# Kernel optimization log

Measured on AMD Instinct MI355X. Metric: run time of the kernel, lower is better.

Reference implementation:

```python
import jax, jax.numpy as jnp
import numpy as np

Q, N_EMBED, DIM = 4, 1024, 256
B, S = 8, 2048


def setup_inputs() -> dict:
    key = jax.random.key(0)
    k1, k2 = jax.random.split(key)
    x = jax.random.normal(k1, (B, S, DIM), dtype=jnp.float32)
    codebooks = jax.random.normal(k2, (Q, N_EMBED, DIM), dtype=jnp.float32)
    return {"x": x, "codebooks": codebooks}


def _vq_lookup(flat, embed):
    # flat: [M, D], embed: [K, D]
    dist = (jnp.sum(flat * flat, axis=-1, keepdims=True)
            - 2.0 * flat @ embed.T
            + jnp.sum(embed * embed, axis=-1))
    idx = jnp.argmin(dist, axis=-1)          # [M]
    quantize = embed[idx]                    # gather: [M, D]
    return quantize, idx


def reference(x, codebooks):
    sg = jax.lax.stop_gradient
    b, s, d = x.shape
    num_q = codebooks.shape[0]
    residual = x
    quantized_output = jnp.zeros_like(x)
    all_indices, all_losses = [], []
    for i in range(num_q):  # small fixed loop over quantizers
        flat = residual.reshape(-1, d)
        q, idx = _vq_lookup(flat, codebooks[i])
        q = q.reshape(b, s, d)
        # commitment loss: mse(sg(quantize), input)
        loss = jnp.mean((sg(q) - residual) ** 2)
        # straight-through estimator
        q_st = residual + sg(q - residual)
        residual = residual - q_st
        quantized_output = quantized_output + q_st
        all_indices.append(idx.reshape(b, s))
        all_losses.append(loss)
    return quantized_output, jnp.stack(all_indices), jnp.stack(all_losses)
```

## Files before the change

kernel.cpp:

```cpp
#include <hip/hip_runtime.h>

#define QQ   4
#define NE   1024
#define DIMD 256
#define MM   16384
#define TM   32
#define NW   16
#define CAP  32

typedef short v8s __attribute__((ext_vector_type(8)));
typedef float v4f __attribute__((ext_vector_type(4)));


__device__ __forceinline__ unsigned short f2bf(float f) {
  unsigned u = __float_as_uint(f);
  return (unsigned short)((u + 0x7FFFu + ((u >> 16) & 1u)) >> 16);
}

__device__ __forceinline__ float np_sumsq_256_x32(const float* __restrict__ p,
                                                  int j) {
  const int bi = j >> 4, L = j & 15;
  const float* q = p + bi * 128 + L;
  float s0 = __fmul_rn(q[0], q[0]);
  float s1 = __fmul_rn(q[16], q[16]);
  float s2 = __fmul_rn(q[32], q[32]);
  float s3 = __fmul_rn(q[48], q[48]);
  float s4 = __fmul_rn(q[64], q[64]);
  float s5 = __fmul_rn(q[80], q[80]);
  float s6 = __fmul_rn(q[96], q[96]);
  float s7 = __fmul_rn(q[112], q[112]);
  float w = __fadd_rn(__fadd_rn(__fadd_rn(s0, s1), __fadd_rn(s2, s3)),
                      __fadd_rn(__fadd_rn(s4, s5), __fadd_rn(s6, s7)));
  float u  = __fadd_rn(w,  __shfl_down(w, 8, 64));
  float t  = __fadd_rn(u,  __shfl_down(u, 4, 64));
  float r2 = __fadd_rn(t,  __shfl_down(t, 2, 64));
  float bb = __fadd_rn(r2, __shfl_down(r2, 1, 64));
  return __fadd_rn(bb, __shfl_down(bb, 16, 64));
}

__device__ __forceinline__ float np_dist_f4(const float* __restrict__ xp,
                                            const float* __restrict__ ep,
                                            float a, float b) {
  float m = 0.f;
  #pragma unroll 16
  for (int d4 = 0; d4 < DIMD / 4; ++d4) {
    const float4 xv = *(const float4*)(xp + d4 * 4);
    const float4 ev = *(const float4*)(ep + d4 * 4);
    m = fmaf(xv.x, ev.x, m);
    m = fmaf(xv.y, ev.y, m);
    m = fmaf(xv.z, ev.z, m);
    m = fmaf(xv.w, ev.w, m);
  }
  return __fadd_rn(__fsub_rn(a, __fmul_rn(2.0f, m)), b);
}

__global__ __launch_bounds__(256) void k_prep(const float* __restrict__ cb,
                                              unsigned short* __restrict__ cb16,
                                              float* __restrict__ bK,
                                              double* __restrict__ lossP,
                                              unsigned* __restrict__ done) {
  const int g = blockIdx.x * 256 + threadIdx.x;
  {
    const int i = g * 4;
    float4 f = *(const float4*)(cb + i);
    unsigned short t[4] = {f2bf(f.x), f2bf(f.y), f2bf(f.z), f2bf(f.w)};
    *(short4*)(cb16 + i) = *(short4*)t;
  }
  if (g < QQ * NE * 32) {
    const int row = g >> 5, j = g & 31;
    float b = np_sumsq_256_x32(cb + (size_t)row * DIMD, j);
    if (j == 0) bK[row] = b;
  }
  if (g < QQ * 64) lossP[g] = 0.0;
  if (g == 0) *done = 0u;
}

__global__ __launch_bounds__(1024, 4) void k_fused(
    const float* __restrict__ x,
    const unsigned short* __restrict__ cb16a,
    const float* __restrict__ cba,
    const float* __restrict__ bKa,
    double* __restrict__ lossP,
    unsigned* __restrict__ doneCnt,
    float* __restrict__ out_q,
    float* __restrict__ idx_out,
    float* __restrict__ out_loss) {
  __shared__ float residF[TM][DIMD + 4];
  __shared__ unsigned short sX[TM][DIMD + 8];
  __shared__ float  sBK[NE];
  __shared__ float  av_s[TM];
  __shared__ float  candD[TM][NW];
  __shared__ float  thrS[TM];
  __shared__ int    cnt[TM];
  __shared__ int    candL[TM][CAP];
  __shared__ float  dcD[TM][CAP];
  __shared__ int    bcode[TM];
  __shared__ float  fwD[NW];
  __shared__ int    fwI[NW];
  __shared__ double lossW[NW];

  const int tid  = threadIdx.x;
  const int lane = tid & 63;
  const int wv   = tid >> 6;
  const int rowBase = blockIdx.x * TM;
  const int r32 = tid >> 5;
  const int j32 = tid & 31;
  const int d0  = j32 * 8;
  const int m16  = lane & 15;
  const int quad = lane >> 4;

  {
    const float* xp = x + (size_t)(rowBase + r32) * DIMD + d0;
    *(float4*)&residF[r32][d0]     = *(const float4*)xp;
    *(float4*)&residF[r32][d0 + 4] = *(const float4*)(xp + 4);
  }
  __syncthreads();

  #pragma unroll 1
  for (int qi = 0; qi < QQ; ++qi) {
    const unsigned short* cb16 = cb16a + (size_t)qi * NE * DIMD;
    const float* cb = cba + (size_t)qi * NE * DIMD;
    const float* bK = bKa + (size_t)qi * NE;

    {
      float av = np_sumsq_256_x32(&residF[r32][0], j32);
      if (j32 == 0) av_s[r32] = av;
    }
    if (tid < TM) cnt[tid] = 0;
    if (tid < NE) sBK[tid] = bK[tid];
    {
      const float* rp = &residF[r32][d0];
      const float4 f0 = *(const float4*)rp;
      const float4 f1 = *(const float4*)(rp + 4);
      unsigned short t[8] = {f2bf(f0.x), f2bf(f0.y), f2bf(f0.z), f2bf(f0.w),
                             f2bf(f1.x), f2bf(f1.y), f2bf(f1.z), f2bf(f1.w)};
      *(v8s*)&sX[r32][d0] = *(v8s*)t;
    }
    __syncthreads();

    float bmx;
    {
      float bm = sBK[lane];
      #pragma unroll
      for (int t = 1; t < 16; ++t) bm = fmaxf(bm, sBK[lane + t * 64]);
      #pragma unroll
      for (int off = 32; off; off >>= 1) bm = fmaxf(bm, __shfl_xor(bm, off, 64));
      bmx = bm;
    }

    v4f acc[2][4];
    #pragma unroll
    for (int mt = 0; mt < 2; ++mt)
      #pragma unroll
      for (int ct = 0; ct < 4; ++ct) acc[mt][ct] = (v4f)(0.f);
    const unsigned short* bptr =
        cb16 + ((size_t)(wv * 64 + m16)) * DIMD + quad * 8;
    #pragma unroll
    for (int kc = 0; kc < 8; ++kc) {
      v8s bfr[4];
      #pragma unroll
      for (int ct = 0; ct < 4; ++ct)
        bfr[ct] = *(const v8s*)(bptr + (size_t)ct * 16 * DIMD + kc * 32);
      v8s a0 = *(const v8s*)&sX[m16][kc * 32 + quad * 8];
      v8s a1 = *(const v8s*)&sX[16 + m16][kc * 32 + quad * 8];
      #pragma unroll
      for (int ct = 0; ct < 4; ++ct) {
        acc[0][ct] = __builtin_amdgcn_mfma_f32_16x16x32_bf16(a0, bfr[ct], acc[0][ct], 0, 0, 0);
        acc[1][ct] = __builtin_amdgcn_mfma_f32_16x16x32_bf16(a1, bfr[ct], acc[1][ct], 0, 0, 0);
      }
    }

    float av8[2][4];
    #pragma unroll
    for (int mt = 0; mt < 2; ++mt)
      #pragma unroll
      for (int v = 0; v < 4; ++v) av8[mt][v] = av_s[mt * 16 + quad * 4 + v];
    #pragma unroll
    for (int ct = 0; ct < 4; ++ct) {
      const float bv = sBK[wv * 64 + ct * 16 + m16];
      #pragma unroll
      for (int mt = 0; mt < 2; ++mt)
        #pragma unroll
        for (int v = 0; v < 4; ++v)
          acc[mt][ct][v] = av8[mt][v] - 2.0f * acc[mt][ct][v] + bv;
    }

    #pragma unroll
    for (int mt = 0; mt < 2; ++mt) {
      float vmin[4];
      #pragma unroll
      for (int v = 0; v < 4; ++v) {
        vmin[v] = acc[mt][0][v];
        #pragma unroll
        for (int ct = 1; ct < 4; ++ct) vmin[v] = fminf(vmin[v], acc[mt][ct][v]);
        #pragma unroll
        for (int off = 1; off < 16; off <<= 1)
          vmin[v] = fminf(vmin[v], __shfl_xor(vmin[v], off, 64));
      }
      if (m16 == 0) {
        #pragma unroll
        for (int v = 0; v < 4; ++v) candD[mt * 16 + quad * 4 + v][wv] = vmin[v];
      }
    }
    __syncthreads();
    if (tid < TM) {
      float bd = candD[tid][0];
      #pragma unroll
      for (int w = 1; w < NW; ++w) bd = fminf(bd, candD[tid][w]);
      thrS[tid] = bd + 0.03125f * sqrtf(av_s[tid] * bmx) + 0.1f;
    }
    __syncthreads();

    #pragma unroll
    for (int ct = 0; ct < 4; ++ct) {
      const int code = wv * 64 + ct * 16 + m16;
      #pragma unroll
      for (int mt = 0; mt < 2; ++mt) {
        #pragma unroll
        for (int v = 0; v < 4; ++v) {
          const int row = mt * 16 + quad * 4 + v;
          if (acc[mt][ct][v] <= thrS[row]) {
            int pos = atomicAdd(&cnt[row], 1);
            if (pos < CAP) candL[row][pos] = code;
          }
        }
      }
    }
    __syncthreads();

    {
      const int n = (cnt[r32] <= CAP) ? cnt[r32] : 0;
      if (j32 < n) {
        const int code = candL[r32][j32];
        dcD[r32][j32] = np_dist_f4(&residF[r32][0], cb + (size_t)code * DIMD,
                                   av_s[r32], sBK[code]);
      }
    }
    __syncthreads();

    for (int r = 0; r < TM; ++r) {
      if (cnt[r] > CAP) {
        const float* xp = &residF[r][0];
        const float a = av_s[r];
        float d1 = np_dist_f4(xp, cb + (size_t)tid * DIMD, a, sBK[tid]);
        int i1 = tid;
        #pragma unroll
        for (int off = 32; off; off >>= 1) {
          float vd = __shfl_xor(d1, off, 64);
          int vi = __shfl_xor(i1, off, 64);
          if (vd < d1 || (vd == d1 && vi < i1)) { d1 = vd; i1 = vi; }
        }
        if (lane == 0) { fwD[wv] = d1; fwI[wv] = i1; }
        __syncthreads();
        if (tid == 0) {
          float bd = fwD[0];
          int bi = fwI[0];
          #pragma unroll
          for (int w = 1; w < NW; ++w) {
            if (fwD[w] < bd || (fwD[w] == bd && fwI[w] < bi)) {
              bd = fwD[w]; bi = fwI[w];
            }
          }
          bcode[r] = bi;
        }
        __syncthreads();
      }
    }

    if (tid < TM) {
      if (cnt[tid] <= CAP) {
        float bd = 3.4e38f;
        int bi = 0x7fffffff;
        for (int ci = 0; ci < cnt[tid]; ++ci) {
          float d = dcD[tid][ci];
          int code = candL[tid][ci];
          if (d < bd || (d == bd && code < bi)) { bd = d; bi = code; }
        }
        bcode[tid] = bi;
      }
      idx_out[(size_t)qi * MM + rowBase + tid] = (float)bcode[tid];
    }
    __syncthreads();

    const int codeB = bcode[r32];
    double lsum = 0.0;
    #pragma unroll
    for (int h = 0; h < 2; ++h) {
      const int d = d0 + h * 4;
      const float4 ev = *(const float4*)(cb + (size_t)codeB * DIMD + d);
      const float4 rv = *(const float4*)&residF[r32][d];
      float t0 = __fsub_rn(ev.x, rv.x), u0 = __fadd_rn(rv.x, t0);
      float t1 = __fsub_rn(ev.y, rv.y), u1 = __fadd_rn(rv.y, t1);
      float t2 = __fsub_rn(ev.z, rv.z), u2 = __fadd_rn(rv.z, t2);
      float t3 = __fsub_rn(ev.w, rv.w), u3 = __fadd_rn(rv.w, t3);
      *(float4*)&residF[r32][d] =
          make_float4(__fsub_rn(rv.x, u0), __fsub_rn(rv.y, u1),
                      __fsub_rn(rv.z, u2), __fsub_rn(rv.w, u3));
      lsum += (double)__fmul_rn(t0, t0) + (double)__fmul_rn(t1, t1) +
              (double)__fmul_rn(t2, t2) + (double)__fmul_rn(t3, t3);
    }
    #pragma unroll
    for (int off = 32; off; off >>= 1) lsum += __shfl_xor(lsum, off, 64);
    if (lane == 0) lossW[wv] = lsum;
    __syncthreads();
    if (tid == 0) {
      double s = 0.0;
      #pragma unroll
      for (int w = 0; w < NW; ++w) s += lossW[w];
      atomicAdd(lossP + (size_t)qi * 64 + (blockIdx.x & 63), s);
    }
  }

  {
    const float* xp = x + (size_t)(rowBase + r32) * DIMD + d0;
    float* op = out_q + (size_t)(rowBase + r32) * DIMD + d0;
    const float4 a0 = *(const float4*)xp;
    const float4 a1 = *(const float4*)(xp + 4);
    const float4 b0 = *(const float4*)&residF[r32][d0];
    const float4 b1 = *(const float4*)&residF[r32][d0 + 4];
    *(float4*)op = make_float4(__fsub_rn(a0.x, b0.x), __fsub_rn(a0.y, b0.y),
                               __fsub_rn(a0.z, b0.z), __fsub_rn(a0.w, b0.w));
    *(float4*)(op + 4) = make_float4(__fsub_rn(a1.x, b1.x), __fsub_rn(a1.y, b1.y),
                                     __fsub_rn(a1.z, b1.z), __fsub_rn(a1.w, b1.w));
  }

  __syncthreads();
  if (tid == 0) {
    __threadfence();
    unsigned old = atomicAdd(doneCnt, 1u);
    cnt[0] = (old == (unsigned)(gridDim.x - 1)) ? 1 : 0;
  }
  __syncthreads();
  if (cnt[0] && tid < 64) {
    const int qi2 = tid >> 4;
    double s = 0.0;
    #pragma unroll
    for (int i = 0; i < 4; ++i)
      s += atomicAdd(lossP + (size_t)qi2 * 64 + (tid & 15) * 4 + i, 0.0);
    #pragma unroll
    for (int off = 8; off; off >>= 1) s += __shfl_down(s, off, 16);
    if ((tid & 15) == 0)
      out_loss[qi2] = (float)(s * (1.0 / (double)((size_t)MM * DIMD)));
  }
}

extern "C" void kernel_launch(void* const* d_in, const int* in_sizes, int n_in,
                              void* d_out, int out_size, void* d_ws, size_t ws_size,
                              hipStream_t stream) {
  const float* x = (const float*)d_in[0];
  const float* cb = (const float*)d_in[1];
  float* ws = (float*)d_ws;
  unsigned short* cb16 = (unsigned short*)ws;
  float* bK = ws + 524288;
  double* lossP = (double*)(ws + 528384);
  unsigned* done = (unsigned*)(ws + 528896);

  float* out = (float*)d_out;
  float* out_idx = out + (size_t)MM * DIMD;
  float* out_loss = out_idx + (size_t)QQ * MM;

  k_prep<<<dim3(1024), dim3(256), 0, stream>>>(cb, cb16, bK, lossP, done);
  k_fused<<<dim3(MM / TM), dim3(1024), 0, stream>>>(x, cb16, cb, bK, lossP,
                                                    done, out, out_idx, out_loss);
}
```

Before: 344.6 us.

## Split fused VQ kernel into per-quantizer prefilter and rerank kernels

Replaces the single fused kernel, which looped over the four quantizers with the residual kept in LDS, with separate launches for each quantizer. A bf16 MFMA prefilter kernel writes candidate lists to global scratch, and a wave-per-row rerank kernel does exact fp32 distances, updates the residual in global memory and accumulates the loss. Final output and loss reduction move to small separate kernels, and the prep kernel now also copies x into the residual buffer. The aim is to remove the serialized per-row full-scan fallback and the block-wide syncs inside the fused loop. In exchange it adds launch overhead and global-memory round trips for the residual and candidates.

```diff
diff --git a/kernel.cpp b/kernel.cpp
--- a/kernel.cpp
+++ b/kernel.cpp
@@ -42,7 +42,7 @@
                                             const float* __restrict__ ep,
                                             float a, float b) {
   float m = 0.f;
-  #pragma unroll 16
+  #pragma unroll 8
   for (int d4 = 0; d4 < DIMD / 4; ++d4) {
     const float4 xv = *(const float4*)(xp + d4 * 4);
     const float4 ev = *(const float4*)(ep + d4 * 4);
@@ -55,37 +55,51 @@
 }
 
 __global__ __launch_bounds__(256) void k_prep(const float* __restrict__ cb,
+                                              const float* __restrict__ x,
                                               unsigned short* __restrict__ cb16,
                                               float* __restrict__ bK,
-                                              double* __restrict__ lossP,
-                                              unsigned* __restrict__ done) {
-  const int g = blockIdx.x * 256 + threadIdx.x;
-  {
-    const int i = g * 4;
-    float4 f = *(const float4*)(cb + i);
-    unsigned short t[4] = {f2bf(f.x), f2bf(f.y), f2bf(f.z), f2bf(f.w)};
-    *(short4*)(cb16 + i) = *(short4*)t;
-  }
-  if (g < QQ * NE * 32) {
-    const int row = g >> 5, j = g & 31;
-    float b = np_sumsq_256_x32(cb + (size_t)row * DIMD, j);
-    if (j == 0) bK[row] = b;
-  }
-  if (g < QQ * 64) lossP[g] = 0.0;
-  if (g == 0) *done = 0u;
-}
-
-__global__ __launch_bounds__(1024, 4) void k_fused(
-    const float* __restrict__ x,
-    const unsigned short* __restrict__ cb16a,
-    const float* __restrict__ cba,
-    const float* __restrict__ bKa,
-    double* __restrict__ lossP,
-    unsigned* __restrict__ doneCnt,
-    float* __restrict__ out_q,
-    float* __restrict__ idx_out,
-    float* __restrict__ out_loss) {
-  __shared__ float residF[TM][DIMD + 4];
+                                              float* __restrict__ resid,
+                                              double* __restrict__ lossP) {
+  __shared__ float rowS[8][256];
+  const int t = threadIdx.x;
+  const size_t base = (size_t)blockIdx.x * 2048;
+  {
+    const float4* src = (const float4*)(cb + base);
+    float4* dst = (float4*)rowS;
+    dst[t] = src[t];
+    dst[t + 256] = src[t + 256];
+  }
+  __syncthreads();
+  {
+    const int r = t >> 5, j = t & 31;
+    float b = np_sumsq_256_x32(&rowS[r][0], j);
+    if (j == 0) bK[blockIdx.x * 8 + r] = b;
+  }
+  {
+    const float* p = &((const float*)rowS)[t * 8];
+    unsigned short o[8];
+    #pragma unroll
+    for (int k = 0; k < 8; ++k) o[k] = f2bf(p[k]);
+    *(v8s*)(cb16 + base + (size_t)t * 8) = *(v8s*)o;
+  }
+  {
+    const float4* xs = (const float4*)x;
+    float4* rd = (float4*)resid;
+    const int gt = blockIdx.x * 256 + t;
+    #pragma unroll
+    for (int k = 0; k < 8; ++k) rd[gt + k * 131072] = xs[gt + k * 131072];
+  }
+  if (blockIdx.x == 0) lossP[t] = 0.0;
+}
+
+__global__ __launch_bounds__(1024, 2) void k_pref(
+    const float* __restrict__ resid,
+    const unsigned short* __restrict__ cb16,
+    const float* __restrict__ bK,
+    float* __restrict__ avS,
+    int*   __restrict__ cntS,
+    int*   __restrict__ candS) {
+  __shared__ float residS[TM][DIMD + 4];
   __shared__ unsigned short sX[TM][DIMD + 8];
   __shared__ float  sBK[NE];
   __shared__ float  av_s[TM];
@@ -93,11 +107,6 @@
   __shared__ float  thrS[TM];
   __shared__ int    cnt[TM];
   __shared__ int    candL[TM][CAP];
-  __shared__ float  dcD[TM][CAP];
-  __shared__ int    bcode[TM];
-  __shared__ float  fwD[NW];
-  __shared__ int    fwI[NW];
-  __shared__ double lossW[NW];
 
   const int tid  = threadIdx.x;
   const int lane = tid & 63;
@@ -110,237 +119,216 @@
   const int quad = lane >> 4;
 
   {
-    const float* xp = x + (size_t)(rowBase + r32) * DIMD + d0;
-    *(float4*)&residF[r32][d0]     = *(const float4*)xp;
-    *(float4*)&residF[r32][d0 + 4] = *(const float4*)(xp + 4);
-  }
-  __syncthreads();
-
-  #pragma unroll 1
-  for (int qi = 0; qi < QQ; ++qi) {
-    const unsigned short* cb16 = cb16a + (size_t)qi * NE * DIMD;
-    const float* cb = cba + (size_t)qi * NE * DIMD;
-    const float* bK = bKa + (size_t)qi * NE;
-
-    {
-      float av = np_sumsq_256_x32(&residF[r32][0], j32);
-      if (j32 == 0) av_s[r32] = av;
-    }
-    if (tid < TM) cnt[tid] = 0;
-    if (tid < NE) sBK[tid] = bK[tid];
-    {
-      const float* rp = &residF[r32][d0];
-      const float4 f0 = *(const float4*)rp;
-      const float4 f1 = *(const float4*)(rp + 4);
-      unsigned short t[8] = {f2bf(f0.x), f2bf(f0.y), f2bf(f0.z), f2bf(f0.w),
-                             f2bf(f1.x), f2bf(f1.y), f2bf(f1.z), f2bf(f1.w)};
-      *(v8s*)&sX[r32][d0] = *(v8s*)t;
-    }
-    __syncthreads();
-
-    float bmx;
-    {
-      float bm = sBK[lane];
-      #pragma unroll
-      for (int t = 1; t < 16; ++t) bm = fmaxf(bm, sBK[lane + t * 64]);
-      #pragma unroll
-      for (int off = 32; off; off >>= 1) bm = fmaxf(bm, __shfl_xor(bm, off, 64));
-      bmx = bm;
-    }
-
-    v4f acc[2][4];
+    const float4* src = (const float4*)(resid + (size_t)rowBase * DIMD);
+    #pragma unroll
+    for (int k = 0; k < 2; ++k) {
+      const int i = tid + k * 1024;
+      const int row = i >> 6, col = (i & 63) << 2;
+      *(float4*)&residS[row][col] = src[i];
+    }
+  }
+  sBK[tid] = bK[tid];
+  __syncthreads();
+
+  {
+    float av = np_sumsq_256_x32(&residS[r32][0], j32);
+    if (j32 == 0) av_s[r32] = av;
+  }
+  if (tid < TM) cnt[tid] = 0;
+  {
+    const float* rp = &residS[r32][d0];
+    const float4 f0 = *(const float4*)rp;
+    const float4 f1 = *(const float4*)(rp + 4);
+    unsigned short t[8] = {f2bf(f0.x), f2bf(f0.y), f2bf(f0.z), f2bf(f0.w),
+                           f2bf(f1.x), f2bf(f1.y), f2bf(f1.z), f2bf(f1.w)};
+    *(v8s*)&sX[r32][d0] = *(v8s*)t;
+  }
+  __syncthreads();
+
+  float bmx;
+  {
+    float bm = sBK[lane];
+    #pragma unroll
+    for (int t = 1; t < 16; ++t) bm = fmaxf(bm, sBK[lane + t * 64]);
+    #pragma unroll
+    for (int off = 32; off; off >>= 1) bm = fmaxf(bm, __shfl_xor(bm, off, 64));
+    bmx = bm;
+  }
+
+  v4f acc[2][4];
+  #pragma unroll
+  for (int mt = 0; mt < 2; ++mt)
+    #pragma unroll
+    for (int ct = 0; ct < 4; ++ct) acc[mt][ct] = (v4f)(0.f);
+  const unsigned short* bptr =
+      cb16 + ((size_t)(wv * 64 + m16)) * DIMD + quad * 8;
+  #pragma unroll
+  for (int kc = 0; kc < 8; ++kc) {
+    v8s bfr[4];
+    #pragma unroll
+    for (int ct = 0; ct < 4; ++ct)
+      bfr[ct] = *(const v8s*)(bptr + (size_t)ct * 16 * DIMD + kc * 32);
+    v8s a0 = *(const v8s*)&sX[m16][kc * 32 + quad * 8];
+    v8s a1 = *(const v8s*)&sX[16 + m16][kc * 32 + quad * 8];
+    #pragma unroll
+    for (int ct = 0; ct < 4; ++ct) {
+      acc[0][ct] = __builtin_amdgcn_mfma_f32_16x16x32_bf16(a0, bfr[ct], acc[0][ct], 0, 0, 0);
+      acc[1][ct] = __builtin_amdgcn_mfma_f32_16x16x32_bf16(a1, bfr[ct], acc[1][ct], 0, 0, 0);
+    }
+  }
+
+  float av8[2][4];
+  #pragma unroll
+  for (int mt = 0; mt < 2; ++mt)
+    #pragma unroll
+    for (int v = 0; v < 4; ++v) av8[mt][v] = av_s[mt * 16 + quad * 4 + v];
+  #pragma unroll
+  for (int ct = 0; ct < 4; ++ct) {
+    const float bv = sBK[wv * 64 + ct * 16 + m16];
     #pragma unroll
     for (int mt = 0; mt < 2; ++mt)
       #pragma unroll
-      for (int ct = 0; ct < 4; ++ct) acc[mt][ct] = (v4f)(0.f);
-    const unsigned short* bptr =
-        cb16 + ((size_t)(wv * 64 + m16)) * DIMD + quad * 8;
-    #pragma unroll
-    for (int kc = 0; kc < 8; ++kc) {
-      v8s bfr[4];
-      #pragma unroll
-      for (int ct = 0; ct < 4; ++ct)
-        bfr[ct] = *(const v8s*)(bptr + (size_t)ct * 16 * DIMD + kc * 32);
-      v8s a0 = *(const v8s*)&sX[m16][kc * 32 + quad * 8];
-      v8s a1 = *(const v8s*)&sX[16 + m16][kc * 32 + quad * 8];
-      #pragma unroll
-      for (int ct = 0; ct < 4; ++ct) {
-        acc[0][ct] = __builtin_amdgcn_mfma_f32_16x16x32_bf16(a0, bfr[ct], acc[0][ct], 0, 0, 0);
-        acc[1][ct] = __builtin_amdgcn_mfma_f32_16x16x32_bf16(a1, bfr[ct], acc[1][ct], 0, 0, 0);
-      }
-    }
-
-    float av8[2][4];
-    #pragma unroll
-    for (int mt = 0; mt < 2; ++mt)
-      #pragma unroll
-      for (int v = 0; v < 4; ++v) av8[mt][v] = av_s[mt * 16 + quad * 4 + v];
-    #pragma unroll
-    for (int ct = 0; ct < 4; ++ct) {
-      const float bv = sBK[wv * 64 + ct * 16 + m16];
-      #pragma unroll
-      for (int mt = 0; mt < 2; ++mt)
-        #pragma unroll
-        for (int v = 0; v < 4; ++v)
-          acc[mt][ct][v] = av8[mt][v] - 2.0f * acc[mt][ct][v] + bv;
-    }
-
+      for (int v = 0; v < 4; ++v)
+        acc[mt][ct][v] = av8[mt][v] - 2.0f * acc[mt][ct][v] + bv;
+  }
+
+  #pragma unroll
+  for (int mt = 0; mt < 2; ++mt) {
+    float vmin[4];
+    #pragma unroll
+    for (int v = 0; v < 4; ++v) {
+      vmin[v] = acc[mt][0][v];
+      #pragma unroll
+      for (int ct = 1; ct < 4; ++ct) vmin[v] = fminf(vmin[v], acc[mt][ct][v]);
+      #pragma unroll
+      for (int off = 1; off < 16; off <<= 1)
+        vmin[v] = fminf(vmin[v], __shfl_xor(vmin[v], off, 64));
+    }
+    if (m16 == 0) {
+      #pragma unroll
+      for (int v = 0; v < 4; ++v) candD[mt * 16 + quad * 4 + v][wv] = vmin[v];
+    }
+  }
+  __syncthreads();
+  if (tid < TM) {
+    float bd = candD[tid][0];
+    #pragma unroll
+    for (int w = 1; w < NW; ++w) bd = fminf(bd, candD[tid][w]);
+    thrS[tid] = bd + 0.03125f * sqrtf(av_s[tid] * bmx) + 0.1f;
+  }
+  __syncthreads();
+
+  #pragma unroll
+  for (int ct = 0; ct < 4; ++ct) {
+    const int code = wv * 64 + ct * 16 + m16;
     #pragma unroll
     for (int mt = 0; mt < 2; ++mt) {
-      float vmin[4];
       #pragma unroll
       for (int v = 0; v < 4; ++v) {
-        vmin[v] = acc[mt][0][v];
-        #pragma unroll
-        for (int ct = 1; ct < 4; ++ct) vmin[v] = fminf(vmin[v], acc[mt][ct][v]);
-        #pragma unroll
-        for (int off = 1; off < 16; off <<= 1)
-          vmin[v] = fminf(vmin[v], __shfl_xor(vmin[v], off, 64));
-      }
-      if (m16 == 0) {
-        #pragma unroll
-        for (int v = 0; v < 4; ++v) candD[mt * 16 + quad * 4 + v][wv] = vmin[v];
-      }
-    }
-    __syncthreads();
-    if (tid < TM) {
-      float bd = candD[tid][0];
-      #pragma unroll
-      for (int w = 1; w < NW; ++w) bd = fminf(bd, candD[tid][w]);
-      thrS[tid] = bd + 0.03125f * sqrtf(av_s[tid] * bmx) + 0.1f;
-    }
-    __syncthreads();
-
-    #pragma unroll
-    for (int ct = 0; ct < 4; ++ct) {
-      const int code = wv * 64 + ct * 16 + m16;
-      #pragma unroll
-      for (int mt = 0; mt < 2; ++mt) {
-        #pragma unroll
-        for (int v = 0; v < 4; ++v) {
-          const int row = mt * 16 + quad * 4 + v;
-          if (acc[mt][ct][v] <= thrS[row]) {
-            int pos = atomicAdd(&cnt[row], 1);
-            if (pos < CAP) candL[row][pos] = code;
-          }
+        const int row = mt * 16 + quad * 4 + v;
+        if (acc[mt][ct][v] <= thrS[row]) {
+          int pos = atomicAdd(&cnt[row], 1);
+          if (pos < CAP) candL[row][pos] = code;
         }
       }
     }
-    __syncthreads();
-
-    {
-      const int n = (cnt[r32] <= CAP) ? cnt[r32] : 0;
-      if (j32 < n) {
-        const int code = candL[r32][j32];
-        dcD[r32][j32] = np_dist_f4(&residF[r32][0], cb + (size_t)code * DIMD,
-                                   av_s[r32], sBK[code]);
-      }
-    }
-    __syncthreads();
-
-    for (int r = 0; r < TM; ++r) {
-      if (cnt[r] > CAP) {
-        const float* xp = &residF[r][0];
-        const float a = av_s[r];
-        float d1 = np_dist_f4(xp, cb + (size_t)tid * DIMD, a, sBK[tid]);
-        int i1 = tid;
-        #pragma unroll
-        for (int off = 32; off; off >>= 1) {
-          float vd = __shfl_xor(d1, off, 64);
-          int vi = __shfl_xor(i1, off, 64);
-          if (vd < d1 || (vd == d1 && vi < i1)) { d1 = vd; i1 = vi; }
-        }
-        if (lane == 0) { fwD[wv] = d1; fwI[wv] = i1; }
-        __syncthreads();
-        if (tid == 0) {
-          float bd = fwD[0];
-          int bi = fwI[0];
-          #pragma unroll
-          for (int w = 1; w < NW; ++w) {
-            if (fwD[w] < bd || (fwD[w] == bd && fwI[w] < bi)) {
-              bd = fwD[w]; bi = fwI[w];
-            }
-          }
-          bcode[r] = bi;
-        }
-        __syncthreads();
-      }
-    }
-
-    if (tid < TM) {
-      if (cnt[tid] <= CAP) {
-        float bd = 3.4e38f;
-        int bi = 0x7fffffff;
-        for (int ci = 0; ci < cnt[tid]; ++ci) {
-          float d = dcD[tid][ci];
-          int code = candL[tid][ci];
-          if (d < bd || (d == bd && code < bi)) { bd = d; bi = code; }
-        }
-        bcode[tid] = bi;
-      }
-      idx_out[(size_t)qi * MM + rowBase + tid] = (float)bcode[tid];
-    }
-    __syncthreads();
-
-    const int codeB = bcode[r32];
-    double lsum = 0.0;
-    #pragma unroll
-    for (int h = 0; h < 2; ++h) {
-      const int d = d0 + h * 4;
-      const float4 ev = *(const float4*)(cb + (size_t)codeB * DIMD + d);
-      const float4 rv = *(const float4*)&residF[r32][d];
-      float t0 = __fsub_rn(ev.x, rv.x), u0 = __fadd_rn(rv.x, t0);
-      float t1 = __fsub_rn(ev.y, rv.y), u1 = __fadd_rn(rv.y, t1);
-      float t2 = __fsub_rn(ev.z, rv.z), u2 = __fadd_rn(rv.z, t2);
-      float t3 = __fsub_rn(ev.w, rv.w), u3 = __fadd_rn(rv.w, t3);
-      *(float4*)&residF[r32][d] =
-          make_float4(__fsub_rn(rv.x, u0), __fsub_rn(rv.y, u1),
-                      __fsub_rn(rv.z, u2), __fsub_rn(rv.w, u3));
-      lsum += (double)__fmul_rn(t0, t0) + (double)__fmul_rn(t1, t1) +
-              (double)__fmul_rn(t2, t2) + (double)__fmul_rn(t3, t3);
-    }
-    #pragma unroll
-    for (int off = 32; off; off >>= 1) lsum += __shfl_xor(lsum, off, 64);
-    if (lane == 0) lossW[wv] = lsum;
-    __syncthreads();
-    if (tid == 0) {
-      double s = 0.0;
-      #pragma unroll
-      for (int w = 0; w < NW; ++w) s += lossW[w];
-      atomicAdd(lossP + (size_t)qi * 64 + (blockIdx.x & 63), s);
-    }
-  }
-
-  {
-    const float* xp = x + (size_t)(rowBase + r32) * DIMD + d0;
-    float* op = out_q + (size_t)(rowBase + r32) * DIMD + d0;
-    const float4 a0 = *(const float4*)xp;
-    const float4 a1 = *(const float4*)(xp + 4);
-    const float4 b0 = *(const float4*)&residF[r32][d0];
-    const float4 b1 = *(const float4*)&residF[r32][d0 + 4];
-    *(float4*)op = make_float4(__fsub_rn(a0.x, b0.x), __fsub_rn(a0.y, b0.y),
-                               __fsub_rn(a0.z, b0.z), __fsub_rn(a0.w, b0.w));
-    *(float4*)(op + 4) = make_float4(__fsub_rn(a1.x, b1.x), __fsub_rn(a1.y, b1.y),
-                                     __fsub_rn(a1.z, b1.z), __fsub_rn(a1.w, b1.w));
-  }
-
-  __syncthreads();
-  if (tid == 0) {
-    __threadfence();
-    unsigned old = atomicAdd(doneCnt, 1u);
-    cnt[0] = (old == (unsigned)(gridDim.x - 1)) ? 1 : 0;
-  }
-  __syncthreads();
-  if (cnt[0] && tid < 64) {
-    const int qi2 = tid >> 4;
+  }
+  __syncthreads();
+
+  if (tid < TM) {
+    cntS[rowBase + tid] = cnt[tid];
+    avS[rowBase + tid] = av_s[tid];
+  }
+  candS[(size_t)(rowBase + r32) * CAP + j32] = candL[r32][j32];
+}
+
+__global__ __launch_bounds__(256, 4) void k_rank(
+    float* __restrict__ resid,
+    const float* __restrict__ cb,
+    const float* __restrict__ bK,
+    const float* __restrict__ avS,
+    const int*   __restrict__ cntS,
+    const int*   __restrict__ candS,
+    float* __restrict__ idx_out,
+    double* __restrict__ lossP) {
+  const int tid  = threadIdx.x;
+  const int lane = tid & 63;
+  const int wv   = tid >> 6;
+  const int half = lane >> 5;
+  const int l32  = lane & 31;
+  const int row  = blockIdx.x * 8 + wv * 2 + half;
+  const float* xp = resid + (size_t)row * DIMD;
+  const float a = avS[row];
+  const int cntv = cntS[row];
+  const int n = (cntv <= CAP) ? cntv : 0;
+
+  float bd = 3.4e38f;
+  int bi = 0x7fffffff;
+  if (l32 < n) {
+    const int code = candS[(size_t)row * CAP + l32];
+    bd = np_dist_f4(xp, cb + (size_t)code * DIMD, a, bK[code]);
+    bi = code;
+  }
+  if (cntv > CAP) {
+    #pragma unroll 1
+    for (int k = 0; k < 32; ++k) {
+      const int code = l32 + k * 32;
+      float d = np_dist_f4(xp, cb + (size_t)code * DIMD, a, bK[code]);
+      if (d < bd || (d == bd && code < bi)) { bd = d; bi = code; }
+    }
+  }
+  #pragma unroll
+  for (int off = 16; off; off >>= 1) {
+    float vd = __shfl_xor(bd, off, 64);
+    int vi = __shfl_xor(bi, off, 64);
+    if (vd < bd || (vd == bd && vi < bi)) { bd = vd; bi = vi; }
+  }
+  if (l32 == 0) idx_out[row] = (float)bi;
+
+  const int codeB = bi;
+  const int d0 = l32 * 8;
+  double lsum = 0.0;
+  #pragma unroll
+  for (int h = 0; h < 2; ++h) {
+    const int d = d0 + h * 4;
+    const float4 ev = *(const float4*)(cb + (size_t)codeB * DIMD + d);
+    const float4 rv = *(const float4*)(xp + d);
+    float t0 = __fsub_rn(ev.x, rv.x), u0 = __fadd_rn(rv.x, t0);
+    float t1 = __fsub_rn(ev.y, rv.y), u1 = __fadd_rn(rv.y, t1);
+    float t2 = __fsub_rn(ev.z, rv.z), u2 = __fadd_rn(rv.z, t2);
+    float t3 = __fsub_rn(ev.w, rv.w), u3 = __fadd_rn(rv.w, t3);
+    *(float4*)(resid + (size_t)row * DIMD + d) =
+        make_float4(__fsub_rn(rv.x, u0), __fsub_rn(rv.y, u1),
+                    __fsub_rn(rv.z, u2), __fsub_rn(rv.w, u3));
+    lsum += (double)__fmul_rn(t0, t0) + (double)__fmul_rn(t1, t1) +
+            (double)__fmul_rn(t2, t2) + (double)__fmul_rn(t3, t3);
+  }
+  #pragma unroll
+  for (int off = 32; off; off >>= 1) lsum += __shfl_xor(lsum, off, 64);
+  if (lane == 0) atomicAdd(lossP + (blockIdx.x & 63), lsum);
+}
+
+__global__ __launch_bounds__(256) void k_final(const float* __restrict__ x,
+                                               const float* __restrict__ resid,
+                                               float* __restrict__ out_q) {
+  size_t i = (size_t)blockIdx.x * blockDim.x + threadIdx.x;
+  const size_t n4 = (size_t)MM * DIMD / 4;
+  const float4* xs = (const float4*)x;
+  const float4* rd = (const float4*)resid;
+  float4* q = (float4*)out_q;
+  for (size_t p = i; p < n4; p += (size_t)gridDim.x * blockDim.x) {
+    float4 a = xs[p], b = rd[p];
+    q[p] = make_float4(__fsub_rn(a.x, b.x), __fsub_rn(a.y, b.y),
+                       __fsub_rn(a.z, b.z), __fsub_rn(a.w, b.w));
+  }
+}
+
+__global__ __launch_bounds__(64) void k_loss(const double* __restrict__ lossP,
+                                             float* __restrict__ out_loss) {
+  if (threadIdx.x < QQ) {
     double s = 0.0;
-    #pragma unroll
-    for (int i = 0; i < 4; ++i)
-      s += atomicAdd(lossP + (size_t)qi2 * 64 + (tid & 15) * 4 + i, 0.0);
-    #pragma unroll
-    for (int off = 8; off; off >>= 1) s += __shfl_down(s, off, 16);
-    if ((tid & 15) == 0)
-      out_loss[qi2] = (float)(s * (1.0 / (double)((size_t)MM * DIMD)));
+    for (int i = 0; i < 64; ++i) s += lossP[(size_t)threadIdx.x * 64 + i];
+    out_loss[threadIdx.x] = (float)(s * (1.0 / (double)((size_t)MM * DIMD)));
   }
 }
 
@@ -353,13 +341,27 @@
   unsigned short* cb16 = (unsigned short*)ws;
   float* bK = ws + 524288;
   double* lossP = (double*)(ws + 528384);
-  unsigned* done = (unsigned*)(ws + 528896);
+  float* resid = ws + 528896;
 
   float* out = (float*)d_out;
   float* out_idx = out + (size_t)MM * DIMD;
   float* out_loss = out_idx + (size_t)QQ * MM;
 
-  k_prep<<<dim3(1024), dim3(256), 0, stream>>>(cb, cb16, bK, lossP, done);
-  k_fused<<<dim3(MM / TM), dim3(1024), 0, stream>>>(x, cb16, cb, bK, lossP,
-                                                    done, out, out_idx, out_loss);
-}
+  int*   candS = (int*)out;
+  int*   cntS  = (int*)(out + 524288);
+  float* avS   = out + 540672;
+
+  k_prep<<<dim3(QQ * NE / 8), dim3(256), 0, stream>>>(cb, x, cb16, bK, resid,
+                                                      lossP);
+  for (int qi = 0; qi < QQ; ++qi) {
+    k_pref<<<dim3(MM / TM), dim3(1024), 0, stream>>>(
+        resid, cb16 + (size_t)qi * NE * DIMD, bK + (size_t)qi * NE,
+        avS, cntS, candS);
+    k_rank<<<dim3(MM / 8), dim3(256), 0, stream>>>(
+        resid, cb + (size_t)qi * NE * DIMD, bK + (size_t)qi * NE,
+        avS, cntS, candS, out_idx + (size_t)qi * MM,
+        lossP + (size_t)qi * 64);
+  }
+  k_final<<<dim3(2048), dim3(256), 0, stream>>>(x, resid, out);
+  k_loss<<<dim3(1), dim3(64), 0, stream>>>(lossP, out_loss);
+}
```

New measurement: 411.5 us. 1.19x slower.
